# Optimization experiments

Hardware: AMD Instinct MI355X
Metric: run time of the kernel (lower is better)

Reference implementation:

```python
import jax, jax.numpy as jnp
import numpy as np

B, S, L = 256, 2048, 64  # batch, seq_len, label_size (= num_labels + 2)
START, END = L - 2, L - 1


def setup_inputs() -> dict:
    key = jax.random.key(0)
    k1, k2, k3, k4 = jax.random.split(key, 4)
    logits = jax.random.normal(k1, (B, S, L), dtype=jnp.float32)
    # pad_logits: <SOS>/<EOS> score columns are -100
    logits = logits.at[:, :, START:].set(-100.0)
    transition = jax.random.normal(k2, (L, L), dtype=jnp.float32)
    # CRF.initialize(): nothing transitions into end-as-source / out of start-as-target
    transition = transition.at[:, END].set(-100.0)
    transition = transition.at[START, :].set(-100.0)
    labels = jax.random.randint(k3, (B, S), 0, L - 2, dtype=jnp.int32)
    lens = jnp.maximum(jax.random.randint(k4, (B,), 1, S + 1, dtype=jnp.int32), 1)
    return {"logits": logits, "transition": transition, "labels": labels, "lens": lens}


def _loglik(logits, transition, labels, lens):
    Bc, Sc, Lc = logits.shape
    dt = logits.dtype
    mask_s = (jnp.arange(Sc)[None, :] < lens[:, None])  # [B,S] valid-token mask

    # ---- gold unary score: sum_t logits[b, t, labels[b,t]] over valid t ----
    unary = jnp.take_along_axis(logits, labels[..., None].astype(jnp.int32), axis=2)[..., 0]
    gold_unary = jnp.sum(unary * mask_s.astype(dt), axis=1)  # [B]

    # ---- gold binary score: transition[to, from] along extended label path ----
    lab_ext = jnp.concatenate(
        [jnp.full((Bc, 1), START, labels.dtype), labels, jnp.full((Bc, 1), END, labels.dtype)],
        axis=1,
    )  # [B, S+2]
    m_ext = jnp.arange(Sc + 2)[None, :] < (lens + 1)[:, None]
    lab_ext = jnp.where(m_ext, lab_ext, END)  # positions past lens become <EOS>
    trn_scr = transition[lab_ext[:, 1:], lab_ext[:, :-1]]  # [B, S+1]
    m_trn = (jnp.arange(Sc + 1)[None, :] < (lens + 1)[:, None]).astype(dt)
    gold_binary = jnp.sum(trn_scr * m_trn, axis=1)  # [B]
    gold = gold_unary + gold_binary

    # ---- norm score: forward algorithm (log-semiring scan over time) ----
    alpha0 = jnp.full((Bc, Lc), -100.0, dtype=dt).at[:, START].set(0.0)

    def step(alpha, inp):
        logit, active = inp  # logit: [B,L], active: [B]
        # mat[b, to, frm] = logit[b,to] + alpha[b,frm] + transition[to,frm]
        mat = logit[:, :, None] + alpha[:, None, :] + transition[None, :, :]
        alpha_nxt = jax.nn.logsumexp(mat, axis=2)  # [B,L]
        alpha = jnp.where(active[:, None], alpha_nxt, alpha)
        return alpha, None

    alpha, _ = jax.lax.scan(step, alpha0, (jnp.swapaxes(logits, 0, 1), mask_s.T))
    norm = jax.nn.logsumexp(alpha + transition[END][None, :], axis=1)  # [B]

    return gold - norm


def reference(logits, transition, labels, lens):
    return _loglik(logits, transition, labels, lens)
```

## Files before the change

### kernel.cpp

```cpp
#include <hip/hip_runtime.h>


#define Bsz 256
#define Ssz 2048
#define START_ 62
#define END_ 63
#define PSTRIDE 36

typedef __attribute__((ext_vector_type(2))) _Float16 half2v;
typedef __attribute__((ext_vector_type(8))) _Float16 half8;
typedef __attribute__((ext_vector_type(16))) float f32x16;

__device__ __forceinline__ unsigned pack_pkrtz(float a, float b) {
    auto h = __builtin_amdgcn_cvt_pkrtz(a, b);
    return __builtin_bit_cast(unsigned, h);
}

__device__ __forceinline__ float dot2h(unsigned a, unsigned b, float c) {
#if __has_builtin(__builtin_amdgcn_fdot2)
    return __builtin_amdgcn_fdot2(__builtin_bit_cast(half2v, a),
                                  __builtin_bit_cast(half2v, b), c, false);
#else
    half2v ha = __builtin_bit_cast(half2v, a);
    half2v hb = __builtin_bit_cast(half2v, b);
    c = __builtin_fmaf((float)ha.x, (float)hb.x, c);
    return __builtin_fmaf((float)ha.y, (float)hb.y, c);
#endif
}

__device__ __forceinline__ float wave_sum(float v) {
#pragma unroll
    for (int m = 32; m >= 1; m >>= 1) v += __shfl_xor(v, m, 64);
    return v;
}

#define CRF_STEP(LG)                                                           \
    {                                                                          \
        const float l_ = __builtin_amdgcn_exp2f((LG) * L2E);                   \
        const int nbi_ = __builtin_amdgcn_update_dpp(                          \
            0, __float_as_int(E), 0xB1, 0xf, 0xf, true);                       \
        const unsigned packed_ = pack_pkrtz(E, __int_as_float(nbi_));          \
        float c0 = 0.f, c1 = 0.f, c2 = 0.f, c3 = 0.f;                          \
        float c4 = 0.f, c5 = 0.f, c6 = 0.f, c7 = 0.f;                          \
        _Pragma("unroll")                                                      \
        for (int k8 = 0; k8 < 8; ++k8) {                                       \
            const uint4 q_ = q[k8];                                            \
            const unsigned t0 = (unsigned)__builtin_amdgcn_readlane(           \
                (int)packed_, 8 * k8 + 0);                                     \
            const unsigned t1 = (unsigned)__builtin_amdgcn_readlane(           \
                (int)packed_, 8 * k8 + 2);                                     \
            const unsigned t2 = (unsigned)__builtin_amdgcn_readlane(           \
                (int)packed_, 8 * k8 + 4);                                     \
            const unsigned t3 = (unsigned)__builtin_amdgcn_readlane(           \
                (int)packed_, 8 * k8 + 6);                                     \
            if (k8 & 1) {                                                      \
                c4 = dot2h(t0, q_.x, c4);                                      \
                c5 = dot2h(t1, q_.y, c5);                                      \
                c6 = dot2h(t2, q_.z, c6);                                      \
                c7 = dot2h(t3, q_.w, c7);                                      \
            } else {                                                           \
                c0 = dot2h(t0, q_.x, c0);                                      \
                c1 = dot2h(t1, q_.y, c1);                                      \
                c2 = dot2h(t2, q_.z, c2);                                      \
                c3 = dot2h(t3, q_.w, c3);                                      \
            }                                                                  \
        }                                                                      \
        const float y_ = ((c0 + c1) + (c2 + c3)) + ((c4 + c5) + (c6 + c7));    \
        const float Ey_ = y_ * l_;                                             \
        const int pb_ = __builtin_amdgcn_readlane(__float_as_int(Ey_), 0);     \
        const int ee_ = (pb_ >> 23) & 0xff;                                    \
        const float sc_ = __int_as_float((244 - ee_) << 23);                   \
        E = Ey_ * sc_;                                                         \
        D += ee_ - 117;                                                        \
    }

#define LOAD_QBLOCK()                                                          \
    {                                                                          \
        unsigned off_ = (unsigned)(lane * (PSTRIDE * 4));                      \
        asm volatile("" : "+v"(off_));                                         \
        const uint4* prow_ = (const uint4*)((const char*)Psh + off_);          \
        _Pragma("unroll")                                                      \
        for (int k8 = 0; k8 < 8; ++k8) q[k8] = prow_[k8];                      \
    }

__global__ __launch_bounds__(64)
__attribute__((amdgpu_waves_per_eu(1, 1)))
void crf_kernel(const float* __restrict__ logits,
                const float* __restrict__ transition,
                const int* __restrict__ labels,
                const int* __restrict__ lens,
                float* __restrict__ out)
{
    const int b    = blockIdx.x;
    const int lane = threadIdx.x;
    const float L2E = 1.4426950408889634f;
    const float LN2 = 0.6931471805599453f;

    __shared__ unsigned Psh[64 * PSTRIDE];

    const int len = lens[b];
    const float* lrow = logits + (size_t)b * (Ssz * 64);

#pragma unroll
    for (int k = 0; k < 32; ++k) {
        float p0 = __builtin_amdgcn_exp2f(transition[lane * 64 + 2 * k]     * L2E);
        float p1 = __builtin_amdgcn_exp2f(transition[lane * 64 + 2 * k + 1] * L2E);
        Psh[lane * PSTRIDE + k] = pack_pkrtz(p0, p1);
    }
    asm volatile("s_waitcnt lgkmcnt(0)" ::: "memory");

    float E = (lane == START_) ? 1.0f : 0.0f;
    int   D = 0;

    float lgb[8];
#pragma unroll
    for (int d = 0; d < 8; ++d) {
        int s0 = (d < len) ? d : (len - 1);
        lgb[d] = lrow[s0 * 64 + lane];
    }

    uint4 q[8];
    const int len8 = len & ~7;
    for (int s = 0; s < len8; s += 8) {
        LOAD_QBLOCK();
#pragma unroll
        for (int d = 0; d < 8; ++d) {
            const float lg = lgb[d];
            int pf = s + 8 + d;
            pf = (pf < len) ? pf : (len - 1);
            lgb[d] = lrow[pf * 64 + lane];
            CRF_STEP(lg);
        }
    }
    const int rem = len - len8;
    if (rem) {
        LOAD_QBLOCK();
        for (int d = 0; d < rem; ++d) {
            const float lg = lgb[d];
            CRF_STEP(lg);
        }
    }

    const float Pend = __builtin_amdgcn_exp2f(transition[END_ * 64 + lane] * L2E);
    const float tot  = wave_sum(E * Pend);
    const float norm = LN2 * ((float)D + __builtin_amdgcn_logf(tot));

    const int* lab = labels + (size_t)b * Ssz;
    float g = 0.0f;
    for (int s = lane; s < len; s += 64) {
        const int l1 = lab[s];
        const int l0 = (s == 0) ? START_ : lab[s - 1];
        g += lrow[s * 64 + l1] + transition[l1 * 64 + l0];
    }
    if (lane == 0) g += transition[END_ * 64 + lab[len - 1]];
    const float gold = wave_sum(g);

    if (lane == 0) out[b] = gold - norm;
}


#define MF16(Aop, Bop, Cop) \
    __builtin_amdgcn_mfma_f32_32x32x16_f16((Aop), (Bop), (Cop), 0, 0, 0)

#define STEP_COMPUTE(LGA, LGB)                                                 \
    f32x16 a00, a01, a10, a11;                                                 \
    {                                                                          \
        const float ncf_ = -(float)ci;                                         \
        const float lv0_ = __builtin_amdgcn_exp2f(                             \
            __builtin_fmaf((LGA), L2E, ncf_));                                 \
        const float lv1_ = __builtin_amdgcn_exp2f(                             \
            __builtin_fmaf((LGB), L2E, ncf_));                                 \
        D += ci;                                                               \
        const _Float16 h0_ = (_Float16)lv0_;                                   \
        const _Float16 h1_ = (_Float16)lv1_;                                   \
        const half8 sv0_ = {h0_, h0_, h0_, h0_, h0_, h0_, h0_, h0_};           \
        const half8 sv1_ = {h1_, h1_, h1_, h1_, h1_, h1_, h1_, h1_};           \
        half8 A_;                                                              \
        __builtin_amdgcn_s_setprio(1);                                         \
        A_ = __builtin_bit_cast(half8, PF[0][0]) * sv0_;                       \
        a00 = MF16(A_, __builtin_bit_cast(half8, Bf[0][0]), Z);                \
        a01 = MF16(A_, __builtin_bit_cast(half8, Bf[0][1]), Z);                \
        A_ = __builtin_bit_cast(half8, PF[0][1]) * sv0_;                       \
        a00 = MF16(A_, __builtin_bit_cast(half8, Bf[1][0]), a00);              \
        a01 = MF16(A_, __builtin_bit_cast(half8, Bf[1][1]), a01);              \
        A_ = __builtin_bit_cast(half8, PF[0][2]) * sv0_;                       \
        a00 = MF16(A_, __builtin_bit_cast(half8, Bf[2][0]), a00);              \
        a01 = MF16(A_, __builtin_bit_cast(half8, Bf[2][1]), a01);              \
        A_ = __builtin_bit_cast(half8, PF[0][3]) * sv0_;                       \
        a00 = MF16(A_, __builtin_bit_cast(half8, Bf[3][0]), a00);              \
        a01 = MF16(A_, __builtin_bit_cast(half8, Bf[3][1]), a01);              \
        A_ = __builtin_bit_cast(half8, PF[1][0]) * sv1_;                       \
        a10 = MF16(A_, __builtin_bit_cast(half8, Bf[0][0]), Z);                \
        a11 = MF16(A_, __builtin_bit_cast(half8, Bf[0][1]), Z);                \
        A_ = __builtin_bit_cast(half8, PF[1][1]) * sv1_;                       \
        a10 = MF16(A_, __builtin_bit_cast(half8, Bf[1][0]), a10);              \
        a11 = MF16(A_, __builtin_bit_cast(half8, Bf[1][1]), a11);              \
        A_ = __builtin_bit_cast(half8, PF[1][2]) * sv1_;                       \
        a10 = MF16(A_, __builtin_bit_cast(half8, Bf[2][0]), a10);              \
        a11 = MF16(A_, __builtin_bit_cast(half8, Bf[2][1]), a11);              \
        A_ = __builtin_bit_cast(half8, PF[1][3]) * sv1_;                       \
        a10 = MF16(A_, __builtin_bit_cast(half8, Bf[3][0]), a10);              \
        a11 = MF16(A_, __builtin_bit_cast(half8, Bf[3][1]), a11);              \
        __builtin_amdgcn_s_setprio(0);                                         \
        const float t0_ = fmaxf(fmaxf(a00[0], a00[1]), a00[2]);                \
        const float t1_ = fmaxf(fmaxf(a00[3], a00[4]), a00[5]);                \
        const float t2_ = fmaxf(fmaxf(a00[6], a00[7]), a00[8]);                \
        const float t3_ = fmaxf(fmaxf(a00[9], a00[10]), a00[11]);              \
        const float t4_ = fmaxf(fmaxf(a00[12], a00[13]), a00[14]);             \
        const float ma_ = fmaxf(fmaxf(t0_, t1_), t2_);                         \
        const float mb2_ = fmaxf(fmaxf(t3_, t4_), a00[15]);                    \
        const int mb_ = __builtin_amdgcn_readfirstlane(                        \
            __float_as_int(fmaxf(ma_, mb2_)));                                 \
        int cin_ = ((mb_ >> 23) & 0xff) - 121;      \
        cin_ = (cin_ < -60) ? -60 : cin_;                                      \
        ci = (cin_ > 60) ? 60 : cin_;                                          \
    }

#define TILE_TO_FRAGS(ACC, BD0, BD1)                                           \
    {                                                                          \
        (BD0) = make_uint4(pack_pkrtz(ACC[0], ACC[1]),                         \
                           pack_pkrtz(ACC[2], ACC[3]),                         \
                           pack_pkrtz(ACC[4], ACC[5]),                         \
                           pack_pkrtz(ACC[6], ACC[7]));                        \
        (BD1) = make_uint4(pack_pkrtz(ACC[8], ACC[9]),                         \
                           pack_pkrtz(ACC[10], ACC[11]),                       \
                           pack_pkrtz(ACC[12], ACC[13]),                       \
                           pack_pkrtz(ACC[14], ACC[15]));                      \
    }

#define STEP_FULL(LGA, LGB)                                                    \
    {                                                                          \
        STEP_COMPUTE(LGA, LGB);                                                \
        TILE_TO_FRAGS(a00, Bf[0][0], Bf[1][0]);                                \
        TILE_TO_FRAGS(a01, Bf[0][1], Bf[1][1]);                                \
        TILE_TO_FRAGS(a10, Bf[2][0], Bf[3][0]);                                \
        TILE_TO_FRAGS(a11, Bf[2][1], Bf[3][1]);                                \
    }

#define STEP_LAST(LGA, LGB)                                                    \
    {                                                                          \
        STEP_COMPUTE(LGA, LGB);                                                \
        float* gout_ = Gws + (size_t)gslot * 4096;                             \
        _Pragma("unroll")                                                      \
        for (int r = 0; r < 16; ++r) {                                         \
            const int row0_ = (r & 3) + 8 * (r >> 2) + 4 * hi;                 \
            gout_[row0_ * 64 + lo5]             = a00[r];                      \
            gout_[row0_ * 64 + 32 + lo5]        = a01[r];                      \
            gout_[(row0_ + 32) * 64 + lo5]      = a10[r];                      \
            gout_[(row0_ + 32) * 64 + 32 + lo5] = a11[r];                      \
        }                                                                      \
        if (lane == 0) Dws[gslot] = D;                                         \
    }

template<int CHT>
__global__ __launch_bounds__(64)
__attribute__((amdgpu_waves_per_eu(3, 8)))
void crf_chunk(const float* __restrict__ logits,
               const float* __restrict__ transition,
               const int* __restrict__ lens,
               float* __restrict__ Gws,
               int* __restrict__ Dws)
{
    const int NCc  = Ssz / CHT;
    const int idx  = blockIdx.x;
    const int c    = idx >> 8;
    const int b    = ((idx & 255) + 37 * c) & 255;
    const int lane = threadIdx.x;
    const int lo5  = lane & 31;
    const int hi   = lane >> 5;
    const float L2E = 1.4426950408889634f;

    const int len   = lens[b];
    const int s0    = c * CHT;
    const int gslot = b * NCc + c;
    if (s0 >= len) {
        if (lane == 0) Dws[gslot] = 0;
        return;
    }
    const int s1 = (s0 + CHT < len) ? (s0 + CHT) : len;

    uint4 PF[2][4];
#pragma unroll
    for (int m = 0; m < 2; ++m) {
#pragma unroll
        for (int kb = 0; kb < 4; ++kb) {
            const float* tp = transition + (m * 32 + lo5) * 64 + kb * 16 + 4 * hi;
            const float e0 = __builtin_amdgcn_exp2f(tp[0] * L2E);
            const float e1 = __builtin_amdgcn_exp2f(tp[1] * L2E);
            const float e2 = __builtin_amdgcn_exp2f(tp[2] * L2E);
            const float e3 = __builtin_amdgcn_exp2f(tp[3] * L2E);
            const float e4 = __builtin_amdgcn_exp2f(tp[8] * L2E);
            const float e5 = __builtin_amdgcn_exp2f(tp[9] * L2E);
            const float e6 = __builtin_amdgcn_exp2f(tp[10] * L2E);
            const float e7 = __builtin_amdgcn_exp2f(tp[11] * L2E);
            PF[m][kb] = make_uint4(pack_pkrtz(e0, e1), pack_pkrtz(e2, e3),
                                   pack_pkrtz(e4, e5), pack_pkrtz(e6, e7));
        }
    }

    uint4 Bf[4][2];
#pragma unroll
    for (int kb = 0; kb < 4; ++kb) {
#pragma unroll
        for (int nb = 0; nb < 2; ++nb) {
            const int col = nb * 32 + lo5;
            unsigned dw[4];
#pragma unroll
            for (int j = 0; j < 4; ++j) {
                const int k0 = kb * 16 + 4 * hi + (j >> 1) * 8 + (j & 1) * 2;
                const unsigned lo16 = (k0     == col) ? 0x3C00u : 0u;
                const unsigned hi16 = (k0 + 1 == col) ? 0x3C00u : 0u;
                dw[j] = lo16 | (hi16 << 16);
            }
            Bf[kb][nb] = make_uint4(dw[0], dw[1], dw[2], dw[3]);
        }
    }

    float z0 = 0.0f;
    asm volatile("" : "+v"(z0));
    f32x16 Z;
#pragma unroll
    for (int i = 0; i < 16; ++i) Z[i] = z0;

    int D  = 0;
    int ci = 0;

    const float* lrow = logits + (size_t)b * (Ssz * 64);
#define CLMP(x) (((x) < s1) ? (x) : (s1 - 1))

    float pA0, pA1, pA2, pA3, pB0, pB1, pB2, pB3;
    {
        int sI;
        sI = CLMP(s0 + 0); pA0 = lrow[sI * 64 + lo5]; pB0 = lrow[sI * 64 + 32 + lo5];
        sI = CLMP(s0 + 1); pA1 = lrow[sI * 64 + lo5]; pB1 = lrow[sI * 64 + 32 + lo5];
        sI = CLMP(s0 + 2); pA2 = lrow[sI * 64 + lo5]; pB2 = lrow[sI * 64 + 32 + lo5];
        sI = CLMP(s0 + 3); pA3 = lrow[sI * 64 + lo5]; pB3 = lrow[sI * 64 + 32 + lo5];
    }

    const int nfull = (s1 - s0) - 1;
    int t = 0;
    for (; t + 4 <= nfull; t += 4) {
        const int sp = s0 + t + 4;
        const int q0i = CLMP(sp), q1i = CLMP(sp + 1), q2i = CLMP(sp + 2), q3i = CLMP(sp + 3);
        const float nA0 = lrow[q0i * 64 + lo5], nB0 = lrow[q0i * 64 + 32 + lo5];
        const float nA1 = lrow[q1i * 64 + lo5], nB1 = lrow[q1i * 64 + 32 + lo5];
        const float nA2 = lrow[q2i * 64 + lo5], nB2 = lrow[q2i * 64 + 32 + lo5];
        const float nA3 = lrow[q3i * 64 + lo5], nB3 = lrow[q3i * 64 + 32 + lo5];
        STEP_FULL(pA0, pB0);
        STEP_FULL(pA1, pB1);
        STEP_FULL(pA2, pB2);
        STEP_FULL(pA3, pB3);
        pA0 = nA0; pB0 = nB0; pA1 = nA1; pB1 = nB1;
        pA2 = nA2; pB2 = nB2; pA3 = nA3; pB3 = nB3;
    }
    const int r_ = nfull - t;
    if (r_ >= 1) STEP_FULL(pA0, pB0);
    if (r_ >= 2) STEP_FULL(pA1, pB1);
    if (r_ >= 3) STEP_FULL(pA2, pB2);

    float fA = pA0, fB = pB0;
    if (r_ == 1) { fA = pA1; fB = pB1; }
    else if (r_ == 2) { fA = pA2; fB = pB2; }
    else if (r_ == 3) { fA = pA3; fB = pB3; }
    STEP_LAST(fA, fB);
#undef CLMP
}

template<int CHT>
__global__ __launch_bounds__(128)
__attribute__((amdgpu_waves_per_eu(1, 2)))
void crf_combine(const float* __restrict__ logits,
                 const float* __restrict__ transition,
                 const int* __restrict__ labels,
                 const int* __restrict__ lens,
                 const float* __restrict__ Gws,
                 const int* __restrict__ Dws,
                 float* __restrict__ out)
{
    const int NCc  = Ssz / CHT;
    const int b    = blockIdx.x;
    const int wid  = threadIdx.x >> 6;
    const int lane = threadIdx.x & 63;
    const float L2E = 1.4426950408889634f;
    const float LN2 = 0.6931471805599453f;
    const int len = lens[b];
    const float* lrow = logits + (size_t)b * (Ssz * 64);

    __shared__ float s_gold;
    float norm = 0.0f;

    if (wid == 1) {
        const int* lab = labels + (size_t)b * Ssz;
        float g = 0.0f;
#pragma unroll 4
        for (int s = lane; s < len; s += 64) {
            const int l1 = lab[s];
            const int l0 = (s == 0) ? START_ : lab[s - 1];
            g += lrow[s * 64 + l1] + transition[l1 * 64 + l0];
        }
        if (lane == 0) g += transition[END_ * 64 + lab[len - 1]];
        const float gold = wave_sum(g);
        if (lane == 0) s_gold = gold;
    } else {
        float E = (lane == START_) ? 1.0f : 0.0f;
        int Dtot = 0;
#pragma unroll 1
        for (int c = 0; c < NCc; ++c) {
            if (c * CHT >= len) break;
            const float4* g4 =
                (const float4*)(Gws + (size_t)(b * NCc + c) * 4096 + lane * 64);
            float4 gr[16];
#pragma unroll
            for (int jj = 0; jj < 16; ++jj) gr[jj] = g4[jj];

            const int Ei = __float_as_int(E);
            float Ens[4] = {0.f, 0.f, 0.f, 0.f};
#pragma unroll
            for (int gq = 0; gq < 4; ++gq) {
#pragma unroll
                for (int qq = 0; qq < 4; ++qq) {
                    const int jj = 4 * gq + qq;
                    Ens[gq] = __builtin_fmaf(gr[jj].x,
                        __int_as_float(__builtin_amdgcn_readlane(Ei, 4 * jj + 0)), Ens[gq]);
                    Ens[gq] = __builtin_fmaf(gr[jj].y,
                        __int_as_float(__builtin_amdgcn_readlane(Ei, 4 * jj + 1)), Ens[gq]);
                    Ens[gq] = __builtin_fmaf(gr[jj].z,
                        __int_as_float(__builtin_amdgcn_readlane(Ei, 4 * jj + 2)), Ens[gq]);
                    Ens[gq] = __builtin_fmaf(gr[jj].w,
                        __int_as_float(__builtin_amdgcn_readlane(Ei, 4 * jj + 3)), Ens[gq]);
                }
            }
            const float En = (Ens[0] + Ens[1]) + (Ens[2] + Ens[3]);
            Dtot += Dws[b * NCc + c];

            float mxv = En;
#pragma unroll
            for (int m = 32; m >= 1; m >>= 1) mxv = fmaxf(mxv, __shfl_xor(mxv, m, 64));
            const int ee = (__float_as_int(mxv) >> 23) & 0xff;
            const float scn = __int_as_float((254 - ee) << 23);
            E = En * scn;
            Dtot += ee - 127;
        }

        const float Pend = __builtin_amdgcn_exp2f(transition[END_ * 64 + lane] * L2E);
        const float tot  = wave_sum(E * Pend);
        norm = LN2 * ((float)Dtot + __builtin_amdgcn_logf(tot));
    }

    __syncthreads();
    if (wid == 0 && lane == 0) out[b] = s_gold - norm;
}

extern "C" void kernel_launch(void* const* d_in, const int* in_sizes, int n_in,
                              void* d_out, int out_size, void* d_ws, size_t ws_size,
                              hipStream_t stream) {
    const float* logits     = (const float*)d_in[0];
    const float* transition = (const float*)d_in[1];
    const int*   labels     = (const int*)d_in[2];
    const int*   lens       = (const int*)d_in[3];
    float*       out        = (float*)d_out;

    const size_t g16  = (size_t)Bsz * 16 * 4096 * sizeof(float);
    const size_t n16  = g16 + (size_t)Bsz * 16 * sizeof(int);
    const size_t g8   = (size_t)Bsz * 8 * 4096 * sizeof(float);
    const size_t n8   = g8 + (size_t)Bsz * 8 * sizeof(int);

    if (d_ws != nullptr && ws_size >= n16) {
        float* Gws = (float*)d_ws;
        int*   Dws = (int*)((char*)d_ws + g16);
        crf_chunk<128><<<dim3(Bsz * 16), dim3(64), 0, stream>>>(
            logits, transition, lens, Gws, Dws);
        crf_combine<128><<<dim3(Bsz), dim3(128), 0, stream>>>(
            logits, transition, labels, lens, Gws, Dws, out);
    } else if (d_ws != nullptr && ws_size >= n8) {
        float* Gws = (float*)d_ws;
        int*   Dws = (int*)((char*)d_ws + g8);
        crf_chunk<256><<<dim3(Bsz * 8), dim3(64), 0, stream>>>(
            logits, transition, lens, Gws, Dws);
        crf_combine<256><<<dim3(Bsz), dim3(128), 0, stream>>>(
            logits, transition, labels, lens, Gws, Dws, out);
    } else {
        crf_kernel<<<dim3(Bsz), dim3(64), 0, stream>>>(
            logits, transition, labels, lens, out);
    }
}
```

Measured before the change: 306.5 us.

## Split chunk product matrix columns across two waves per block

Each chunk block now runs two waves, and each wave computes only one 32-column half of the 64x64 transfer matrix product, halving the MFMA chain per wave per time step. Each wave keeps its own scale exponent D. The combine kernel reconciles the two per-half exponents by rescaling to the maximum. The aim is to shorten the sequential latency per step and double parallelism. The cost is duplicated exp and A-fragment work in both waves, and possible underflow when the two half exponents differ widely.

Result: slower. 320.6 us (+4.6%).

```diff
diff --git a/kernel.cpp b/kernel.cpp
--- a/kernel.cpp
+++ b/kernel.cpp
@@ -163,7 +163,7 @@
     __builtin_amdgcn_mfma_f32_32x32x16_f16((Aop), (Bop), (Cop), 0, 0, 0)
 
 #define STEP_COMPUTE(LGA, LGB)                                                 \
-    f32x16 a00, a01, a10, a11;                                                 \
+    f32x16 a00, a10;                                                           \
     {                                                                          \
         const float ncf_ = -(float)ci;                                         \
         const float lv0_ = __builtin_amdgcn_exp2f(                             \
@@ -178,29 +178,21 @@
         half8 A_;                                                              \
         __builtin_amdgcn_s_setprio(1);                                         \
         A_ = __builtin_bit_cast(half8, PF[0][0]) * sv0_;                       \
-        a00 = MF16(A_, __builtin_bit_cast(half8, Bf[0][0]), Z);                \
-        a01 = MF16(A_, __builtin_bit_cast(half8, Bf[0][1]), Z);                \
+        a00 = MF16(A_, __builtin_bit_cast(half8, Bf[0]), Z);                   \
         A_ = __builtin_bit_cast(half8, PF[0][1]) * sv0_;                       \
-        a00 = MF16(A_, __builtin_bit_cast(half8, Bf[1][0]), a00);              \
-        a01 = MF16(A_, __builtin_bit_cast(half8, Bf[1][1]), a01);              \
+        a00 = MF16(A_, __builtin_bit_cast(half8, Bf[1]), a00);                 \
         A_ = __builtin_bit_cast(half8, PF[0][2]) * sv0_;                       \
-        a00 = MF16(A_, __builtin_bit_cast(half8, Bf[2][0]), a00);              \
-        a01 = MF16(A_, __builtin_bit_cast(half8, Bf[2][1]), a01);              \
+        a00 = MF16(A_, __builtin_bit_cast(half8, Bf[2]), a00);                 \
         A_ = __builtin_bit_cast(half8, PF[0][3]) * sv0_;                       \
-        a00 = MF16(A_, __builtin_bit_cast(half8, Bf[3][0]), a00);              \
-        a01 = MF16(A_, __builtin_bit_cast(half8, Bf[3][1]), a01);              \
+        a00 = MF16(A_, __builtin_bit_cast(half8, Bf[3]), a00);                 \
         A_ = __builtin_bit_cast(half8, PF[1][0]) * sv1_;                       \
-        a10 = MF16(A_, __builtin_bit_cast(half8, Bf[0][0]), Z);                \
-        a11 = MF16(A_, __builtin_bit_cast(half8, Bf[0][1]), Z);                \
+        a10 = MF16(A_, __builtin_bit_cast(half8, Bf[0]), Z);                   \
         A_ = __builtin_bit_cast(half8, PF[1][1]) * sv1_;                       \
-        a10 = MF16(A_, __builtin_bit_cast(half8, Bf[1][0]), a10);              \
-        a11 = MF16(A_, __builtin_bit_cast(half8, Bf[1][1]), a11);              \
+        a10 = MF16(A_, __builtin_bit_cast(half8, Bf[1]), a10);                 \
         A_ = __builtin_bit_cast(half8, PF[1][2]) * sv1_;                       \
-        a10 = MF16(A_, __builtin_bit_cast(half8, Bf[2][0]), a10);              \
-        a11 = MF16(A_, __builtin_bit_cast(half8, Bf[2][1]), a11);              \
+        a10 = MF16(A_, __builtin_bit_cast(half8, Bf[2]), a10);                 \
         A_ = __builtin_bit_cast(half8, PF[1][3]) * sv1_;                       \
-        a10 = MF16(A_, __builtin_bit_cast(half8, Bf[3][0]), a10);              \
-        a11 = MF16(A_, __builtin_bit_cast(half8, Bf[3][1]), a11);              \
+        a10 = MF16(A_, __builtin_bit_cast(half8, Bf[3]), a10);                 \
         __builtin_amdgcn_s_setprio(0);                                         \
         const float t0_ = fmaxf(fmaxf(a00[0], a00[1]), a00[2]);                \
         const float t1_ = fmaxf(fmaxf(a00[3], a00[4]), a00[5]);                \
@@ -231,30 +223,26 @@
 #define STEP_FULL(LGA, LGB)                                                    \
     {                                                                          \
         STEP_COMPUTE(LGA, LGB);                                                \
-        TILE_TO_FRAGS(a00, Bf[0][0], Bf[1][0]);                                \
-        TILE_TO_FRAGS(a01, Bf[0][1], Bf[1][1]);                                \
-        TILE_TO_FRAGS(a10, Bf[2][0], Bf[3][0]);                                \
-        TILE_TO_FRAGS(a11, Bf[2][1], Bf[3][1]);                                \
+        TILE_TO_FRAGS(a00, Bf[0], Bf[1]);                                      \
+        TILE_TO_FRAGS(a10, Bf[2], Bf[3]);                                      \
     }
 
 #define STEP_LAST(LGA, LGB)                                                    \
     {                                                                          \
         STEP_COMPUTE(LGA, LGB);                                                \
-        float* gout_ = Gws + (size_t)gslot * 4096;                             \
+        float* gout_ = Gws + (size_t)gslot * 4096 + nb * 32;                   \
         _Pragma("unroll")                                                      \
         for (int r = 0; r < 16; ++r) {                                         \
             const int row0_ = (r & 3) + 8 * (r >> 2) + 4 * hi;                 \
-            gout_[row0_ * 64 + lo5]             = a00[r];                      \
-            gout_[row0_ * 64 + 32 + lo5]        = a01[r];                      \
-            gout_[(row0_ + 32) * 64 + lo5]      = a10[r];                      \
-            gout_[(row0_ + 32) * 64 + 32 + lo5] = a11[r];                      \
+            gout_[row0_ * 64 + lo5]        = a00[r];                           \
+            gout_[(row0_ + 32) * 64 + lo5] = a10[r];                           \
         }                                                                      \
-        if (lane == 0) Dws[gslot] = D;                                         \
+        if (lo5 == 0 && hi == 0) Dws[gslot * 2 + nb] = D;                      \
     }
 
 template<int CHT>
-__global__ __launch_bounds__(64)
-__attribute__((amdgpu_waves_per_eu(3, 8)))
+__global__ __launch_bounds__(128)
+__attribute__((amdgpu_waves_per_eu(4, 8)))
 void crf_chunk(const float* __restrict__ logits,
                const float* __restrict__ transition,
                const int* __restrict__ lens,
@@ -265,7 +253,8 @@
     const int idx  = blockIdx.x;
     const int c    = idx >> 8;
     const int b    = ((idx & 255) + 37 * c) & 255;
-    const int lane = threadIdx.x;
+    const int nb   = threadIdx.x >> 6;
+    const int lane = threadIdx.x & 63;
     const int lo5  = lane & 31;
     const int hi   = lane >> 5;
     const float L2E = 1.4426950408889634f;
@@ -274,7 +263,7 @@
     const int s0    = c * CHT;
     const int gslot = b * NCc + c;
     if (s0 >= len) {
-        if (lane == 0) Dws[gslot] = 0;
+        if (lane == 0) Dws[gslot * 2 + nb] = 0;
         return;
     }
     const int s1 = (s0 + CHT < len) ? (s0 + CHT) : len;
@@ -298,22 +287,19 @@
         }
     }
 
-    uint4 Bf[4][2];
+    uint4 Bf[4];
 #pragma unroll
     for (int kb = 0; kb < 4; ++kb) {
-#pragma unroll
-        for (int nb = 0; nb < 2; ++nb) {
-            const int col = nb * 32 + lo5;
-            unsigned dw[4];
-#pragma unroll
-            for (int j = 0; j < 4; ++j) {
-                const int k0 = kb * 16 + 4 * hi + (j >> 1) * 8 + (j & 1) * 2;
-                const unsigned lo16 = (k0     == col) ? 0x3C00u : 0u;
-                const unsigned hi16 = (k0 + 1 == col) ? 0x3C00u : 0u;
-                dw[j] = lo16 | (hi16 << 16);
-            }
-            Bf[kb][nb] = make_uint4(dw[0], dw[1], dw[2], dw[3]);
-        }
+        const int col = nb * 32 + lo5;
+        unsigned dw[4];
+#pragma unroll
+        for (int j = 0; j < 4; ++j) {
+            const int k0 = kb * 16 + 4 * hi + (j >> 1) * 8 + (j & 1) * 2;
+            const unsigned lo16 = (k0     == col) ? 0x3C00u : 0u;
+            const unsigned hi16 = (k0 + 1 == col) ? 0x3C00u : 0u;
+            dw[j] = lo16 | (hi16 << 16);
+        }
+        Bf[kb] = make_uint4(dw[0], dw[1], dw[2], dw[3]);
     }
 
     float z0 = 0.0f;
@@ -430,8 +416,14 @@
                         __int_as_float(__builtin_amdgcn_readlane(Ei, 4 * jj + 3)), Ens[gq]);
                 }
             }
-            const float En = (Ens[0] + Ens[1]) + (Ens[2] + Ens[3]);
-            Dtot += Dws[b * NCc + c];
+            const int D0 = Dws[(b * NCc + c) * 2 + 0];
+            const int D1 = Dws[(b * NCc + c) * 2 + 1];
+            const int Dm = (D0 > D1) ? D0 : D1;
+            const int e0 = 127 + D0 - Dm, e1 = 127 + D1 - Dm;
+            const float sc0 = (e0 > 0) ? __int_as_float(e0 << 23) : 0.0f;
+            const float sc1 = (e1 > 0) ? __int_as_float(e1 << 23) : 0.0f;
+            const float En = (Ens[0] + Ens[1]) * sc0 + (Ens[2] + Ens[3]) * sc1;
+            Dtot += Dm;
 
             float mxv = En;
 #pragma unroll
@@ -461,21 +453,21 @@
     float*       out        = (float*)d_out;
 
     const size_t g16  = (size_t)Bsz * 16 * 4096 * sizeof(float);
-    const size_t n16  = g16 + (size_t)Bsz * 16 * sizeof(int);
+    const size_t n16  = g16 + (size_t)Bsz * 16 * 2 * sizeof(int);
     const size_t g8   = (size_t)Bsz * 8 * 4096 * sizeof(float);
-    const size_t n8   = g8 + (size_t)Bsz * 8 * sizeof(int);
+    const size_t n8   = g8 + (size_t)Bsz * 8 * 2 * sizeof(int);
 
     if (d_ws != nullptr && ws_size >= n16) {
         float* Gws = (float*)d_ws;
         int*   Dws = (int*)((char*)d_ws + g16);
-        crf_chunk<128><<<dim3(Bsz * 16), dim3(64), 0, stream>>>(
+        crf_chunk<128><<<dim3(Bsz * 16), dim3(128), 0, stream>>>(
             logits, transition, lens, Gws, Dws);
         crf_combine<128><<<dim3(Bsz), dim3(128), 0, stream>>>(
             logits, transition, labels, lens, Gws, Dws, out);
     } else if (d_ws != nullptr && ws_size >= n8) {
         float* Gws = (float*)d_ws;
         int*   Dws = (int*)((char*)d_ws + g8);
-        crf_chunk<256><<<dim3(Bsz * 8), dim3(64), 0, stream>>>(
+        crf_chunk<256><<<dim3(Bsz * 8), dim3(128), 0, stream>>>(
             logits, transition, lens, Gws, Dws);
         crf_combine<256><<<dim3(Bsz), dim3(128), 0, stream>>>(
             logits, transition, labels, lens, Gws, Dws, out);
```

## Split CRF scan into 32-step chunks with fp16 tree-merge of transfer matrices

Applied to the files above, without the earlier changes.

Sequence chunks shrink from 128 to 32 steps, giving 64 chunk blocks per batch row. Each chunk stores its 64x64 transfer matrix in fp16 with a block exponent. Six log-depth merge launches then multiply adjacent matrices with MFMA, replacing the sequential combine over chunks. This shortens the serial critical path and raises parallelism. In exchange it adds extra kernel launches, matrix-product work and fp16 rounding at every merge level.

Result: slower. 382.3 us (+24.7%).

```diff
diff --git a/kernel.cpp b/kernel.cpp
--- a/kernel.cpp
+++ b/kernel.cpp
@@ -32,6 +32,11 @@
 #pragma unroll
     for (int m = 32; m >= 1; m >>= 1) v += __shfl_xor(v, m, 64);
     return v;
+}
+
+__device__ __forceinline__ float h16_to_f(unsigned short u) {
+    _Float16 h = __builtin_bit_cast(_Float16, u);
+    return (float)h;
 }
 
 #define CRF_STEP(LG)                                                           \
@@ -237,7 +242,88 @@
         TILE_TO_FRAGS(a11, Bf[2][1], Bf[3][1]);                                \
     }
 
-#define STEP_LAST(LGA, LGB)                                                    \
+#define CHUNK_PROLOGUE()                                                       \
+    uint4 PF[2][4];                                                            \
+    _Pragma("unroll")                                                          \
+    for (int m = 0; m < 2; ++m) {                                              \
+        _Pragma("unroll")                                                      \
+        for (int kb = 0; kb < 4; ++kb) {                                       \
+            const float* tp = transition + (m * 32 + lo5) * 64 + kb * 16 + 4 * hi; \
+            const float e0 = __builtin_amdgcn_exp2f(tp[0] * L2E);              \
+            const float e1 = __builtin_amdgcn_exp2f(tp[1] * L2E);              \
+            const float e2 = __builtin_amdgcn_exp2f(tp[2] * L2E);              \
+            const float e3 = __builtin_amdgcn_exp2f(tp[3] * L2E);              \
+            const float e4 = __builtin_amdgcn_exp2f(tp[8] * L2E);              \
+            const float e5 = __builtin_amdgcn_exp2f(tp[9] * L2E);              \
+            const float e6 = __builtin_amdgcn_exp2f(tp[10] * L2E);             \
+            const float e7 = __builtin_amdgcn_exp2f(tp[11] * L2E);             \
+            PF[m][kb] = make_uint4(pack_pkrtz(e0, e1), pack_pkrtz(e2, e3),     \
+                                   pack_pkrtz(e4, e5), pack_pkrtz(e6, e7));    \
+        }                                                                      \
+    }                                                                          \
+    uint4 Bf[4][2];                                                            \
+    _Pragma("unroll")                                                          \
+    for (int kb = 0; kb < 4; ++kb) {                                           \
+        _Pragma("unroll")                                                      \
+        for (int nb = 0; nb < 2; ++nb) {                                       \
+            const int col = nb * 32 + lo5;                                     \
+            unsigned dw[4];                                                    \
+            _Pragma("unroll")                                                  \
+            for (int j = 0; j < 4; ++j) {                                      \
+                const int k0 = kb * 16 + 4 * hi + (j >> 1) * 8 + (j & 1) * 2;  \
+                const unsigned lo16 = (k0     == col) ? 0x3C00u : 0u;          \
+                const unsigned hi16 = (k0 + 1 == col) ? 0x3C00u : 0u;          \
+                dw[j] = lo16 | (hi16 << 16);                                   \
+            }                                                                  \
+            Bf[kb][nb] = make_uint4(dw[0], dw[1], dw[2], dw[3]);               \
+        }                                                                      \
+    }                                                                          \
+    float z0 = 0.0f;                                                           \
+    asm volatile("" : "+v"(z0));                                               \
+    f32x16 Z;                                                                  \
+    _Pragma("unroll")                                                          \
+    for (int i = 0; i < 16; ++i) Z[i] = z0;                                    \
+    int D  = 0;                                                                \
+    int ci = 0;
+
+#define CHUNK_LOOP(LASTMACRO)                                                  \
+    const float* lrow = logits + (size_t)b * (Ssz * 64);                       \
+    float pA0, pA1, pA2, pA3, pB0, pB1, pB2, pB3;                              \
+    {                                                                          \
+        int sI;                                                                \
+        sI = CLMP(s0 + 0); pA0 = lrow[sI * 64 + lo5]; pB0 = lrow[sI * 64 + 32 + lo5]; \
+        sI = CLMP(s0 + 1); pA1 = lrow[sI * 64 + lo5]; pB1 = lrow[sI * 64 + 32 + lo5]; \
+        sI = CLMP(s0 + 2); pA2 = lrow[sI * 64 + lo5]; pB2 = lrow[sI * 64 + 32 + lo5]; \
+        sI = CLMP(s0 + 3); pA3 = lrow[sI * 64 + lo5]; pB3 = lrow[sI * 64 + 32 + lo5]; \
+    }                                                                          \
+    const int nfull = (s1 - s0) - 1;                                           \
+    int t = 0;                                                                 \
+    for (; t + 4 <= nfull; t += 4) {                                           \
+        const int sp = s0 + t + 4;                                             \
+        const int q0i = CLMP(sp), q1i = CLMP(sp + 1), q2i = CLMP(sp + 2), q3i = CLMP(sp + 3); \
+        const float nA0 = lrow[q0i * 64 + lo5], nB0 = lrow[q0i * 64 + 32 + lo5]; \
+        const float nA1 = lrow[q1i * 64 + lo5], nB1 = lrow[q1i * 64 + 32 + lo5]; \
+        const float nA2 = lrow[q2i * 64 + lo5], nB2 = lrow[q2i * 64 + 32 + lo5]; \
+        const float nA3 = lrow[q3i * 64 + lo5], nB3 = lrow[q3i * 64 + 32 + lo5]; \
+        STEP_FULL(pA0, pB0);                                                   \
+        STEP_FULL(pA1, pB1);                                                   \
+        STEP_FULL(pA2, pB2);                                                   \
+        STEP_FULL(pA3, pB3);                                                   \
+        pA0 = nA0; pB0 = nB0; pA1 = nA1; pB1 = nB1;                            \
+        pA2 = nA2; pB2 = nB2; pA3 = nA3; pB3 = nB3;                            \
+    }                                                                          \
+    const int r_ = nfull - t;                                                  \
+    if (r_ >= 1) STEP_FULL(pA0, pB0);                                          \
+    if (r_ >= 2) STEP_FULL(pA1, pB1);                                          \
+    if (r_ >= 3) STEP_FULL(pA2, pB2);                                          \
+    float fA = pA0, fB = pB0;                                                  \
+    if (r_ == 1) { fA = pA1; fB = pB1; }                                       \
+    else if (r_ == 2) { fA = pA2; fB = pB2; }                                  \
+    else if (r_ == 3) { fA = pA3; fB = pB3; }                                  \
+    LASTMACRO(fA, fB);
+
+
+#define STEP_LAST_F32(LGA, LGB)                                                \
     {                                                                          \
         STEP_COMPUTE(LGA, LGB);                                                \
         float* gout_ = Gws + (size_t)gslot * 4096;                             \
@@ -279,90 +365,9 @@
     }
     const int s1 = (s0 + CHT < len) ? (s0 + CHT) : len;
 
-    uint4 PF[2][4];
-#pragma unroll
-    for (int m = 0; m < 2; ++m) {
-#pragma unroll
-        for (int kb = 0; kb < 4; ++kb) {
-            const float* tp = transition + (m * 32 + lo5) * 64 + kb * 16 + 4 * hi;
-            const float e0 = __builtin_amdgcn_exp2f(tp[0] * L2E);
-            const float e1 = __builtin_amdgcn_exp2f(tp[1] * L2E);
-            const float e2 = __builtin_amdgcn_exp2f(tp[2] * L2E);
-            const float e3 = __builtin_amdgcn_exp2f(tp[3] * L2E);
-            const float e4 = __builtin_amdgcn_exp2f(tp[8] * L2E);
-            const float e5 = __builtin_amdgcn_exp2f(tp[9] * L2E);
-            const float e6 = __builtin_amdgcn_exp2f(tp[10] * L2E);
-            const float e7 = __builtin_amdgcn_exp2f(tp[11] * L2E);
-            PF[m][kb] = make_uint4(pack_pkrtz(e0, e1), pack_pkrtz(e2, e3),
-                                   pack_pkrtz(e4, e5), pack_pkrtz(e6, e7));
-        }
-    }
-
-    uint4 Bf[4][2];
-#pragma unroll
-    for (int kb = 0; kb < 4; ++kb) {
-#pragma unroll
-        for (int nb = 0; nb < 2; ++nb) {
-            const int col = nb * 32 + lo5;
-            unsigned dw[4];
-#pragma unroll
-            for (int j = 0; j < 4; ++j) {
-                const int k0 = kb * 16 + 4 * hi + (j >> 1) * 8 + (j & 1) * 2;
-                const unsigned lo16 = (k0     == col) ? 0x3C00u : 0u;
-                const unsigned hi16 = (k0 + 1 == col) ? 0x3C00u : 0u;
-                dw[j] = lo16 | (hi16 << 16);
-            }
-            Bf[kb][nb] = make_uint4(dw[0], dw[1], dw[2], dw[3]);
-        }
-    }
-
-    float z0 = 0.0f;
-    asm volatile("" : "+v"(z0));
-    f32x16 Z;
-#pragma unroll
-    for (int i = 0; i < 16; ++i) Z[i] = z0;
-
-    int D  = 0;
-    int ci = 0;
-
-    const float* lrow = logits + (size_t)b * (Ssz * 64);
+    CHUNK_PROLOGUE();
 #define CLMP(x) (((x) < s1) ? (x) : (s1 - 1))
-
-    float pA0, pA1, pA2, pA3, pB0, pB1, pB2, pB3;
-    {
-        int sI;
-        sI = CLMP(s0 + 0); pA0 = lrow[sI * 64 + lo5]; pB0 = lrow[sI * 64 + 32 + lo5];
-        sI = CLMP(s0 + 1); pA1 = lrow[sI * 64 + lo5]; pB1 = lrow[sI * 64 + 32 + lo5];
-        sI = CLMP(s0 + 2); pA2 = lrow[sI * 64 + lo5]; pB2 = lrow[sI * 64 + 32 + lo5];
-        sI = CLMP(s0 + 3); pA3 = lrow[sI * 64 + lo5]; pB3 = lrow[sI * 64 + 32 + lo5];
-    }
-
-    const int nfull = (s1 - s0) - 1;
-    int t = 0;
-    for (; t + 4 <= nfull; t += 4) {
-        const int sp = s0 + t + 4;
-        const int q0i = CLMP(sp), q1i = CLMP(sp + 1), q2i = CLMP(sp + 2), q3i = CLMP(sp + 3);
-        const float nA0 = lrow[q0i * 64 + lo5], nB0 = lrow[q0i * 64 + 32 + lo5];
-        const float nA1 = lrow[q1i * 64 + lo5], nB1 = lrow[q1i * 64 + 32 + lo5];
-        const float nA2 = lrow[q2i * 64 + lo5], nB2 = lrow[q2i * 64 + 32 + lo5];
-        const float nA3 = lrow[q3i * 64 + lo5], nB3 = lrow[q3i * 64 + 32 + lo5];
-        STEP_FULL(pA0, pB0);
-        STEP_FULL(pA1, pB1);
-        STEP_FULL(pA2, pB2);
-        STEP_FULL(pA3, pB3);
-        pA0 = nA0; pB0 = nB0; pA1 = nA1; pB1 = nB1;
-        pA2 = nA2; pB2 = nB2; pA3 = nA3; pB3 = nB3;
-    }
-    const int r_ = nfull - t;
-    if (r_ >= 1) STEP_FULL(pA0, pB0);
-    if (r_ >= 2) STEP_FULL(pA1, pB1);
-    if (r_ >= 3) STEP_FULL(pA2, pB2);
-
-    float fA = pA0, fB = pB0;
-    if (r_ == 1) { fA = pA1; fB = pB1; }
-    else if (r_ == 2) { fA = pA2; fB = pB2; }
-    else if (r_ == 3) { fA = pA3; fB = pB3; }
-    STEP_LAST(fA, fB);
+    CHUNK_LOOP(STEP_LAST_F32);
 #undef CLMP
 }
 
@@ -451,6 +456,221 @@
     if (wid == 0 && lane == 0) out[b] = s_gold - norm;
 }
 
+
+#define STEP_LAST_F16(LGA, LGB)                                                \
+    {                                                                          \
+        STEP_COMPUTE(LGA, LGB);                                                \
+        unsigned short* gout_ = G16 + (size_t)gslot * 4096;                    \
+        _Pragma("unroll")                                                      \
+        for (int r = 0; r < 16; ++r) {                                         \
+            const int row0_ = (r & 3) + 8 * (r >> 2) + 4 * hi;                 \
+            gout_[row0_ * 64 + lo5] =                                          \
+                (unsigned short)(pack_pkrtz(a00[r], a00[r]) & 0xffffu);        \
+            gout_[row0_ * 64 + 32 + lo5] =                                     \
+                (unsigned short)(pack_pkrtz(a01[r], a01[r]) & 0xffffu);        \
+            gout_[(row0_ + 32) * 64 + lo5] =                                   \
+                (unsigned short)(pack_pkrtz(a10[r], a10[r]) & 0xffffu);        \
+            gout_[(row0_ + 32) * 64 + 32 + lo5] =                              \
+                (unsigned short)(pack_pkrtz(a11[r], a11[r]) & 0xffffu);        \
+        }                                                                      \
+        if (lane == 0) Dws[gslot] = D;                                         \
+    }
+
+template<int CHT>
+__global__ __launch_bounds__(64)
+__attribute__((amdgpu_waves_per_eu(3, 8)))
+void crf_chunk16(const float* __restrict__ logits,
+                 const float* __restrict__ transition,
+                 const int* __restrict__ lens,
+                 unsigned short* __restrict__ G16,
+                 int* __restrict__ Dws)
+{
+    const int NCc  = Ssz / CHT;
+    const int idx  = blockIdx.x;
+    const int c    = idx >> 8;
+    const int b    = ((idx & 255) + 37 * c) & 255;
+    const int lane = threadIdx.x;
+    const int lo5  = lane & 31;
+    const int hi   = lane >> 5;
+    const float L2E = 1.4426950408889634f;
+
+    const int len   = lens[b];
+    const int s0    = c * CHT;
+    const int gslot = b * NCc + c;
+    if (s0 >= len) {
+        if (lane == 0) Dws[gslot] = (int)0x80000000;
+        return;
+    }
+    const int s1 = (s0 + CHT < len) ? (s0 + CHT) : len;
+
+    CHUNK_PROLOGUE();
+#define CLMP(x) (((x) < s1) ? (x) : (s1 - 1))
+    CHUNK_LOOP(STEP_LAST_F16);
+#undef CLMP
+}
+
+__global__ __launch_bounds__(64)
+__attribute__((amdgpu_waves_per_eu(2, 8)))
+void crf_merge(unsigned short* __restrict__ G16,
+               int* __restrict__ Dws,
+               int lev, int pbLog)
+{
+    const int idx  = blockIdx.x;
+    const int j    = idx & ((1 << pbLog) - 1);
+    const int b    = idx >> pbLog;
+    const int lane = threadIdx.x;
+    const int lo5  = lane & 31;
+    const int hi   = lane >> 5;
+
+    const int aslot  = j << (lev + 1);
+    const int gA     = b * 64 + aslot;
+    const int gB     = gA + (1 << lev);
+
+    const int Db = Dws[gB];
+    if (Db == (int)0x80000000) return;
+    const int Da = Dws[gA];
+
+    const unsigned short* Ra = G16 + (size_t)gA * 4096;
+    const unsigned short* Rb = G16 + (size_t)gB * 4096;
+
+    uint4 PFm[2][4];
+#pragma unroll
+    for (int m = 0; m < 2; ++m) {
+#pragma unroll
+        for (int kb = 0; kb < 4; ++kb) {
+            const unsigned short* bp = Rb + (m * 32 + lo5) * 64 + kb * 16 + 4 * hi;
+            const unsigned d0 = *(const unsigned*)(bp + 0);
+            const unsigned d1 = *(const unsigned*)(bp + 2);
+            const unsigned d2 = *(const unsigned*)(bp + 8);
+            const unsigned d3 = *(const unsigned*)(bp + 10);
+            PFm[m][kb] = make_uint4(d0, d1, d2, d3);
+        }
+    }
+
+    uint4 Bfm[4][2];
+#pragma unroll
+    for (int kb = 0; kb < 4; ++kb) {
+#pragma unroll
+        for (int nb = 0; nb < 2; ++nb) {
+            const int col = nb * 32 + lo5;
+            unsigned dw[4];
+#pragma unroll
+            for (int jd = 0; jd < 4; ++jd) {
+                const int k0 = kb * 16 + 4 * hi + (jd >> 1) * 8 + (jd & 1) * 2;
+                const unsigned lo16 = Ra[k0 * 64 + col];
+                const unsigned hi16 = Ra[(k0 + 1) * 64 + col];
+                dw[jd] = lo16 | (hi16 << 16);
+            }
+            Bfm[kb][nb] = make_uint4(dw[0], dw[1], dw[2], dw[3]);
+        }
+    }
+
+    float z0 = 0.0f;
+    asm volatile("" : "+v"(z0));
+    f32x16 Z;
+#pragma unroll
+    for (int i = 0; i < 16; ++i) Z[i] = z0;
+
+    f32x16 a00, a01, a10, a11;
+    half8 A_;
+    A_ = __builtin_bit_cast(half8, PFm[0][0]);
+    a00 = MF16(A_, __builtin_bit_cast(half8, Bfm[0][0]), Z);
+    a01 = MF16(A_, __builtin_bit_cast(half8, Bfm[0][1]), Z);
+    A_ = __builtin_bit_cast(half8, PFm[0][1]);
+    a00 = MF16(A_, __builtin_bit_cast(half8, Bfm[1][0]), a00);
+    a01 = MF16(A_, __builtin_bit_cast(half8, Bfm[1][1]), a01);
+    A_ = __builtin_bit_cast(half8, PFm[0][2]);
+    a00 = MF16(A_, __builtin_bit_cast(half8, Bfm[2][0]), a00);
+    a01 = MF16(A_, __builtin_bit_cast(half8, Bfm[2][1]), a01);
+    A_ = __builtin_bit_cast(half8, PFm[0][3]);
+    a00 = MF16(A_, __builtin_bit_cast(half8, Bfm[3][0]), a00);
+    a01 = MF16(A_, __builtin_bit_cast(half8, Bfm[3][1]), a01);
+    A_ = __builtin_bit_cast(half8, PFm[1][0]);
+    a10 = MF16(A_, __builtin_bit_cast(half8, Bfm[0][0]), Z);
+    a11 = MF16(A_, __builtin_bit_cast(half8, Bfm[0][1]), Z);
+    A_ = __builtin_bit_cast(half8, PFm[1][1]);
+    a10 = MF16(A_, __builtin_bit_cast(half8, Bfm[1][0]), a10);
+    a11 = MF16(A_, __builtin_bit_cast(half8, Bfm[1][1]), a11);
+    A_ = __builtin_bit_cast(half8, PFm[1][2]);
+    a10 = MF16(A_, __builtin_bit_cast(half8, Bfm[2][0]), a10);
+    a11 = MF16(A_, __builtin_bit_cast(half8, Bfm[2][1]), a11);
+    A_ = __builtin_bit_cast(half8, PFm[1][3]);
+    a10 = MF16(A_, __builtin_bit_cast(half8, Bfm[3][0]), a10);
+    a11 = MF16(A_, __builtin_bit_cast(half8, Bfm[3][1]), a11);
+
+    const float t0 = fmaxf(fmaxf(a00[0], a00[1]), a00[2]);
+    const float t1 = fmaxf(fmaxf(a00[3], a00[4]), a00[5]);
+    const float t2 = fmaxf(fmaxf(a00[6], a00[7]), a00[8]);
+    const float t3 = fmaxf(fmaxf(a00[9], a00[10]), a00[11]);
+    const float t4 = fmaxf(fmaxf(a00[12], a00[13]), a00[14]);
+    const float ma = fmaxf(fmaxf(t0, t1), t2);
+    const float mb2 = fmaxf(fmaxf(t3, t4), a00[15]);
+    const int mb = __builtin_amdgcn_readfirstlane(
+        __float_as_int(fmaxf(ma, mb2)));
+    const int ee = (mb >> 23) & 0xff;
+    const float sc = __int_as_float((248 - ee) << 23);
+
+    unsigned short* gout = G16 + (size_t)gA * 4096;
+#pragma unroll
+    for (int r = 0; r < 16; ++r) {
+        const int row0 = (r & 3) + 8 * (r >> 2) + 4 * hi;
+        gout[row0 * 64 + lo5] =
+            (unsigned short)(pack_pkrtz(a00[r] * sc, 0.f) & 0xffffu);
+        gout[row0 * 64 + 32 + lo5] =
+            (unsigned short)(pack_pkrtz(a01[r] * sc, 0.f) & 0xffffu);
+        gout[(row0 + 32) * 64 + lo5] =
+            (unsigned short)(pack_pkrtz(a10[r] * sc, 0.f) & 0xffffu);
+        gout[(row0 + 32) * 64 + 32 + lo5] =
+            (unsigned short)(pack_pkrtz(a11[r] * sc, 0.f) & 0xffffu);
+    }
+    if (lane == 0) Dws[gA] = Da + Db + (ee - 121);
+}
+
+__global__ __launch_bounds__(128)
+__attribute__((amdgpu_waves_per_eu(1, 2)))
+void crf_combine16(const float* __restrict__ logits,
+                   const float* __restrict__ transition,
+                   const int* __restrict__ labels,
+                   const int* __restrict__ lens,
+                   const unsigned short* __restrict__ G16,
+                   const int* __restrict__ Dws,
+                   float* __restrict__ out)
+{
+    const int b    = blockIdx.x;
+    const int wid  = threadIdx.x >> 6;
+    const int lane = threadIdx.x & 63;
+    const float L2E = 1.4426950408889634f;
+    const float LN2 = 0.6931471805599453f;
+    const int len = lens[b];
+    const float* lrow = logits + (size_t)b * (Ssz * 64);
+
+    __shared__ float s_gold;
+    float norm = 0.0f;
+
+    if (wid == 1) {
+        const int* lab = labels + (size_t)b * Ssz;
+        float g = 0.0f;
+#pragma unroll 4
+        for (int s = lane; s < len; s += 64) {
+            const int l1 = lab[s];
+            const int l0 = (s == 0) ? START_ : lab[s - 1];
+            g += lrow[s * 64 + l1] + transition[l1 * 64 + l0];
+        }
+        if (lane == 0) g += transition[END_ * 64 + lab[len - 1]];
+        const float gold = wave_sum(g);
+        if (lane == 0) s_gold = gold;
+    } else {
+        const int Dg = Dws[b * 64];
+        const float Ei = h16_to_f(G16[(size_t)(b * 64) * 4096 + lane * 64 + START_]);
+        const float Pend = __builtin_amdgcn_exp2f(transition[END_ * 64 + lane] * L2E);
+        const float tot  = wave_sum(Ei * Pend);
+        norm = LN2 * ((float)Dg + __builtin_amdgcn_logf(tot));
+    }
+
+    __syncthreads();
+    if (wid == 0 && lane == 0) out[b] = s_gold - norm;
+}
+
 extern "C" void kernel_launch(void* const* d_in, const int* in_sizes, int n_in,
                               void* d_out, int out_size, void* d_ws, size_t ws_size,
                               hipStream_t stream) {
@@ -460,12 +680,26 @@
     const int*   lens       = (const int*)d_in[3];
     float*       out        = (float*)d_out;
 
+    const size_t gNew = (size_t)Bsz * 64 * 4096 * sizeof(unsigned short);
+    const size_t nNew = gNew + (size_t)Bsz * 64 * sizeof(int);
     const size_t g16  = (size_t)Bsz * 16 * 4096 * sizeof(float);
     const size_t n16  = g16 + (size_t)Bsz * 16 * sizeof(int);
     const size_t g8   = (size_t)Bsz * 8 * 4096 * sizeof(float);
     const size_t n8   = g8 + (size_t)Bsz * 8 * sizeof(int);
 
-    if (d_ws != nullptr && ws_size >= n16) {
+    if (d_ws != nullptr && ws_size >= nNew) {
+        unsigned short* G16 = (unsigned short*)d_ws;
+        int* Dws = (int*)((char*)d_ws + gNew);
+        crf_chunk16<32><<<dim3(Bsz * 64), dim3(64), 0, stream>>>(
+            logits, transition, lens, G16, Dws);
+        for (int lev = 0; lev < 6; ++lev) {
+            const int pbLog = 5 - lev;
+            crf_merge<<<dim3(Bsz << pbLog), dim3(64), 0, stream>>>(
+                G16, Dws, lev, pbLog);
+        }
+        crf_combine16<<<dim3(Bsz), dim3(128), 0, stream>>>(
+            logits, transition, labels, lens, G16, Dws, out);
+    } else if (d_ws != nullptr && ws_size >= n16) {
         float* Gws = (float*)d_ws;
         int*   Dws = (int*)((char*)d_ws + g16);
         crf_chunk<128><<<dim3(Bsz * 16), dim3(64), 0, stream>>>(
```
